# Optimization experiments

Hardware: AMD Instinct MI355X
Metric: run time of the kernel (lower is better)

The kernel has to match this reference:

```python
import jax, jax.numpy as jnp
import numpy as np

G = 8           # graphs
NBG = 1024      # blocks per graph
APB = 4         # atoms per block
NC = 1          # coord channels
HID = 512
ES = 64
K = 9
L = 3
NLVL = 50
NB = G * NBG
NU = NB * APB
NUM_BLOCK, NUM_ATOM, NUM_POS = 25, 16, 16
BIG = 1e9


def _cumsum_ids(seg_lengths, n):
    # faithful to torch: zeros, mark segment starts via cumsum(lengths)[:-1], cumsum
    ids = jnp.zeros((n,), jnp.int32).at[jnp.cumsum(seg_lengths)[:-1]].set(1)
    return jnp.cumsum(ids)


def setup_inputs() -> dict:
    key = jax.random.key(0)
    ks = jax.random.split(key, 18)
    s = 0.02
    return {
        'Z': 3.0 * jax.random.normal(ks[0], (NU, NC, 3), jnp.float32),
        'B': jax.random.randint(ks[1], (NB,), 0, NUM_BLOCK),
        'A': jax.random.randint(ks[2], (NU,), 0, NUM_ATOM),
        'atom_positions': jax.random.randint(ks[3], (NU,), 0, NUM_POS),
        'block_lengths': jnp.full((NB,), APB, jnp.int32),
        'lengths': jnp.full((G,), NBG, jnp.int32),
        'segment_ids': jax.random.randint(ks[4], (NB,), 0, 2),
        'noise': jax.random.normal(ks[5], (NU, NC, 3), jnp.float32),
        'noise_level': jax.random.randint(ks[6], (G,), 0, NLVL),
        'sigmas': jnp.asarray(np.exp(np.linspace(np.log(10.0), np.log(0.01), NLVL)), jnp.float32),
        'atom_emb': s * jax.random.normal(ks[7], (NUM_ATOM, HID), jnp.float32),
        'pos_emb': s * jax.random.normal(ks[8], (NUM_POS, HID), jnp.float32),
        'block_emb': s * jax.random.normal(ks[9], (NUM_BLOCK, HID), jnp.float32),
        'edge_emb': s * jax.random.normal(ks[10], (2, ES), jnp.float32),
        'Wm': s * jax.random.normal(ks[11], (L, HID, HID), jnp.float32),
        'We': s * jax.random.normal(ks[12], (L, ES, HID), jnp.float32),
        'Wu': s * jax.random.normal(ks[13], (L, HID, HID), jnp.float32),
        'wz': s * jax.random.normal(ks[14], (L, HID), jnp.float32),
        'W1': s * jax.random.normal(ks[15], (HID, HID), jnp.float32),
        'b1': jnp.zeros((HID,), jnp.float32),
        'W2': s * jax.random.normal(ks[16], (HID, 1), jnp.float32),
    }


def _forward(Z, B, A, atom_positions, block_lengths, lengths, segment_ids,
             noise, noise_level, sigmas, atom_emb, pos_emb, block_emb, edge_emb,
             Wm, We, Wu, wz, W1, b1, W2):
    nb, nu, g = B.shape[0], A.shape[0], lengths.shape[0]
    nbg, apb = nb // g, nu // nb
    batch_id = _cumsum_ids(lengths, nb)        # [Nb]
    block_id = _cumsum_ids(block_lengths, nu)  # [Nu]

    # perturb: Z + noise * sigma[noise_level[graph]]
    used = sigmas[noise_level][batch_id][block_id]          # [Nu]
    Zp = Z + noise * used[:, None, None]                    # [Nu, NC, 3]

    # block embedding: atom + position + block-type
    H0 = atom_emb[A] + pos_emb[atom_positions] + block_emb[B][block_id]  # [Nu, H]

    # edges: fully connect -> split intra/inter by segment -> knn by min atom-pair distance
    xa = Zp.reshape(g, nbg * apb * NC, 3)
    sq = jnp.sum(xa * xa, axis=-1)
    d2 = sq[:, :, None] + sq[:, None, :] - 2.0 * jnp.einsum('gnd,gmd->gnm', xa, xa)
    D = d2.reshape(g, nbg, apb * NC, nbg, apb * NC).min(axis=(2, 4))     # [g, nbg, nbg]
    seg = segment_ids.reshape(g, nbg)
    same = seg[:, :, None] == seg[:, None, :]
    eye = jnp.eye(nbg, dtype=bool)[None]
    _, idx_intra = jax.lax.top_k(-jnp.where(same & ~eye, D, BIG), K)     # [g, nbg, K]
    _, idx_inter = jax.lax.top_k(-jnp.where(~same, D, BIG), K)
    off = (jnp.arange(g, dtype=jnp.int32) * nbg)[:, None, None]
    dst_loc = jnp.broadcast_to(jnp.arange(nbg, dtype=jnp.int32)[None, :, None] + off, (g, nbg, K))
    src = jnp.concatenate([(idx_intra + off).reshape(-1), (idx_inter + off).reshape(-1)])
    dst = jnp.concatenate([dst_loc.reshape(-1), dst_loc.reshape(-1)])
    eattr = edge_emb[jnp.concatenate([jnp.zeros(g * nbg * K, jnp.int32), jnp.ones(g * nbg * K, jnp.int32)])]

    # encoder (GET surrogate): block-level equivariant message passing
    h = jax.ops.segment_sum(H0, block_id, num_segments=nb) / apb                    # [Nb, H]
    Zb0 = jax.ops.segment_sum(Zp.mean(axis=1), block_id, num_segments=nb) / apb    # [Nb, 3]
    Zb = Zb0
    for l in range(Wm.shape[0]):
        m = jax.nn.silu((h[src] + h[dst]) @ Wm[l] + eattr @ We[l])                  # [E, H]
        h = h + jax.nn.silu(jax.ops.segment_sum(m, dst, num_segments=nb) @ Wu[l])
        coef = jnp.tanh(m @ wz[l])                                                  # [E]
        Zb = Zb + jax.ops.segment_sum((Zb[src] - Zb[dst]) * coef[:, None], dst, num_segments=nb) / (2 * K)
    pred_Z = Zp + (Zb - Zb0)[block_id][:, None, :]
    unit_repr = H0 + h[block_id]
    block_repr = h
    graph_repr = jax.ops.segment_sum(h, batch_id, num_segments=g)

    # energy head: SiLU -> Linear -> SiLU -> Linear(no bias), summed per graph
    e = jax.nn.silu(jax.nn.silu(block_repr) @ W1 + b1) @ W2                         # [Nb, 1]
    pred_energy = jax.ops.segment_sum(e[:, 0], batch_id, num_segments=g)            # [g]

    pred_noise = pred_Z - Zp
    per_unit = jnp.sum((pred_noise - noise) ** 2, axis=(-1, -2))                    # [Nu]
    nl = jax.ops.segment_sum(per_unit, batch_id[block_id], num_segments=g)
    loss = 0.5 * nl.mean()
    return pred_energy, pred_noise, unit_repr, block_repr, graph_repr, loss


def reference(Z, B, A, atom_positions, block_lengths, lengths, segment_ids,
              noise, noise_level, sigmas, atom_emb, pos_emb, block_emb, edge_emb,
              Wm, We, Wu, wz, W1, b1, W2):
    return _forward(Z, B, A, atom_positions, block_lengths, lengths, segment_ids,
                    noise, noise_level, sigmas, atom_emb, pos_emb, block_emb, edge_emb,
                    Wm, We, Wu, wz, W1, b1, W2)
```

## Files before the change

### kernel.cpp

```cpp
#include <hip/hip_runtime.h>
#include <hip/hip_bf16.h>

typedef __bf16 bf16;
typedef __bf16 bf16x2 __attribute__((ext_vector_type(2)));
typedef __bf16 bf16x8 __attribute__((ext_vector_type(8)));
typedef float floatx4 __attribute__((ext_vector_type(4)));

#define NB_ 8192
#define NU_ 32768

__device__ __forceinline__ float silu_f(float x) {
    float e = __expf(-x);
    return x * __builtin_amdgcn_rcpf(1.0f + e);
}

__device__ __forceinline__ float2 unpack_bf2(unsigned v) {
    float2 r;
    r.x = __uint_as_float(v << 16);
    r.y = __uint_as_float(v & 0xFFFF0000u);
    return r;
}

__device__ __forceinline__ void gll16(const bf16* g, bf16* l) {
    __builtin_amdgcn_global_load_lds((const __attribute__((address_space(1))) void*)g,
                                     (__attribute__((address_space(3))) void*)l, 16, 0, 0);
}

__global__ __launch_bounds__(256) void init_kernel(
    const float* __restrict__ Z, const float* __restrict__ noise,
    const int* __restrict__ nl, const float* __restrict__ sig,
    const int* __restrict__ Aarr, const int* __restrict__ posa, const int* __restrict__ Barr,
    const float* __restrict__ atom_emb, const float* __restrict__ pos_emb,
    const float* __restrict__ block_emb,
    const float* __restrict__ edge_emb, const float* __restrict__ We,
    const float* __restrict__ Wm, const float* __restrict__ Wu, const float* __restrict__ W1,
    float* __restrict__ Zp, float* __restrict__ Zb0, float* __restrict__ Zb,
    float* __restrict__ hf, bf16* __restrict__ hb,
    bf16* __restrict__ WmT, bf16* __restrict__ WuT, bf16* __restrict__ W1T,
    float* __restrict__ ebias,
    float* __restrict__ out_gr, float* __restrict__ eblk, float* __restrict__ out_loss)
{
    __shared__ float zsh[12];
    __shared__ float tile[32][33];
    int bid = blockIdx.x, tid = threadIdx.x;
    if (bid < 8192) {
        int b = bid, g = b >> 10;
        if (tid < 12) {
            float sg = sig[nl[g]];
            int idx = b*12 + tid;
            float zp = Z[idx] + noise[idx]*sg;
            Zp[idx] = zp;
            zsh[tid] = zp;
        }
        __syncthreads();
        if (tid < 3) {
            float v = 0.25f*(zsh[tid] + zsh[3+tid] + zsh[6+tid] + zsh[9+tid]);
            Zb0[b*3+tid] = v; Zb[b*3+tid] = v;
        }
        int ai[4], pi[4];
        #pragma unroll
        for (int a = 0; a < 4; a++) { ai[a] = Aarr[b*4+a]*512; pi[a] = posa[b*4+a]*512; }
        int bb = Barr[b]*512;
        #pragma unroll
        for (int cc = 0; cc < 2; cc++) {
            int c = tid + cc*256;
            float s = 0.0f;
            #pragma unroll
            for (int a = 0; a < 4; a++) s += atom_emb[ai[a]+c] + pos_emb[pi[a]+c];
            s = 0.25f*s + block_emb[bb+c];
            hf[(size_t)b*512+c] = s;
            hb[(size_t)b*512+c] = (bf16)s;
        }
        return;
    }
    bid -= 8192;
    if (bid < 1792) {
        int z = bid >> 8, rem = bid & 255;
        int bx = rem & 15, by = rem >> 4;
        int tx = tid & 31, ty = tid >> 5;
        const float* src; bf16* dst;
        if (z < 3)      { src = Wm + (size_t)z*262144;     dst = WmT + (size_t)z*262144; }
        else if (z < 6) { src = Wu + (size_t)(z-3)*262144; dst = WuT + (size_t)(z-3)*262144; }
        else            { src = W1;                        dst = W1T; }
        #pragma unroll
        for (int i = 0; i < 32; i += 8)
            tile[ty+i][tx] = src[(size_t)(by*32+ty+i)*512 + bx*32+tx];
        __syncthreads();
        #pragma unroll
        for (int i = 0; i < 32; i += 8)
            dst[(size_t)(bx*32+ty+i)*512 + by*32+tx] = (bf16)tile[tx][ty+i];
        return;
    }
    bid -= 1792;
    if (bid < 12) {
        int gid = bid*256 + tid;
        int l = gid >> 10, t = (gid >> 9) & 1, c = gid & 511;
        float s = 0.0f;
        #pragma unroll 8
        for (int e = 0; e < 64; e++)
            s += edge_emb[t*64 + e] * We[(size_t)(l*64 + e)*512 + c];
        ebias[gid] = s;
        return;
    }
    bid -= 12;
    int k = bid*256 + tid;
    if (k < 4096) out_gr[k] = 0.0f;
    else if (k < 12288) eblk[k-4096] = 0.0f;
    else if (k == 12288) out_loss[0] = 0.0f;
}

__device__ void knn_body(int kb, const float* __restrict__ Zp, const int* __restrict__ seg,
                         int* __restrict__ nbr) {
    int wid = threadIdx.x >> 6;
    int lane = threadIdx.x & 63;
    int r = ((kb & 7) << 10) + ((kb >> 3) << 2) + wid;
    int g = r >> 10;
    int il = r & 1023;
    int base = g << 10;
    int segr = seg[r];
    float za[4][3];
    #pragma unroll
    for (int a = 0; a < 4; a++)
        #pragma unroll
        for (int d = 0; d < 3; d++)
            za[a][d] = Zp[r*12 + a*3 + d];
    float dist[16];
    unsigned smask = 0;
    #pragma unroll
    for (int t = 0; t < 16; t++) {
        int jb = base + t*64 + lane;
        const float4* p = (const float4*)(Zp + (size_t)jb*12);
        float4 v0 = p[0], v1 = p[1], v2 = p[2];
        float bx[4] = {v0.x, v0.w, v1.z, v2.y};
        float by[4] = {v0.y, v1.x, v1.w, v2.z};
        float bz[4] = {v0.z, v1.y, v2.x, v2.w};
        float dm = 3.0e38f;
        #pragma unroll
        for (int a = 0; a < 4; a++) {
            #pragma unroll
            for (int bq = 0; bq < 4; bq++) {
                float dx = za[a][0]-bx[bq], dy = za[a][1]-by[bq], dz = za[a][2]-bz[bq];
                dm = fminf(dm, dx*dx + dy*dy + dz*dz);
            }
        }
        dist[t] = dm;
        if (seg[jb] == segr) smask |= (1u << t);
    }
    const float INF = 3.0e38f;
    for (int phase = 0; phase < 2; phase++) {
        float wd[16];
        #pragma unroll
        for (int t = 0; t < 16; t++) {
            bool ok = (phase == 0) ? (((smask >> t) & 1u) && (t*64 + lane != il))
                                   : (!((smask >> t) & 1u));
            wd[t] = ok ? dist[t] : INF;
        }
        for (int it = 0; it < 9; it++) {
            float bd = wd[0]; int bt = 0;
            #pragma unroll
            for (int t = 1; t < 16; t++) { if (wd[t] < bd) { bd = wd[t]; bt = t; } }
            float mv = bd;
            #pragma unroll
            for (int off = 32; off >= 1; off >>= 1) mv = fminf(mv, __shfl_xor(mv, off, 64));
            unsigned long long msk = __ballot(bd == mv);
            int wl = __ffsll(msk) - 1;
            int wt = __shfl(bt, wl, 64);
            if (lane == 0) nbr[r*18 + phase*9 + it] = base + wt*64 + wl;
            bool amwin = (lane == wl);
            #pragma unroll
            for (int t = 0; t < 16; t++) if (amwin && t == wt) wd[t] = INF;
        }
    }
}

__device__ void gemm_body(const bf16* __restrict__ A, const bf16* __restrict__ BT,
                          bf16* __restrict__ Pb, float* __restrict__ hf,
                          bf16* __restrict__ hb, bf16* __restrict__ shp,
                          const float* __restrict__ b1, const float* __restrict__ W2,
                          float* __restrict__ eblk,
                          float* __restrict__ Zb, const float* __restrict__ zacc,
                          int mode, int bid)
{
    __shared__ alignas(16) bf16 sA[128*32];
    __shared__ alignas(16) bf16 sB[64*32];
    int mt = bid & 63, nt = bid >> 6;
    int m0 = mt*128, n0 = nt*64;
    int tid = threadIdx.x, lane = tid & 63, w = tid >> 6;
    int wm = w & 1, wn = w >> 1;
    int lm = lane & 15, q = lane >> 4;

    int pA0 = w*128 + lane, pA1 = pA0 + 64, pB = w*64 + lane;
    int rA0 = pA0 >> 2, qA0 = (pA0 & 3) ^ ((rA0 >> 1) & 3);
    int rA1 = pA1 >> 2, qA1 = (pA1 & 3) ^ ((rA1 >> 1) & 3);
    int rB  = pB  >> 2, qB  = (pB  & 3) ^ ((rB  >> 1) & 3);
    const bf16* gA0 = A  + (size_t)(m0 + rA0)*512 + qA0*8;
    const bf16* gA1 = A  + (size_t)(m0 + rA1)*512 + qA1*8;
    const bf16* gB  = BT + (size_t)(n0 + rB )*512 + qB*8;
    bf16* lA0 = sA + (w*128)*8;
    bf16* lA1 = sA + (w*128 + 64)*8;
    bf16* lB  = sB + (w*64)*8;

    int swq = (q ^ ((lm >> 1) & 3)) * 8;
    const bf16* pa[4]; const bf16* pb2[2];
    #pragma unroll
    for (int tm = 0; tm < 4; tm++) pa[tm] = sA + (wm*64 + tm*16 + lm)*32 + swq;
    #pragma unroll
    for (int tn = 0; tn < 2; tn++) pb2[tn] = sB + (wn*32 + tn*16 + lm)*32 + swq;

    floatx4 zv = {0.0f, 0.0f, 0.0f, 0.0f};
    floatx4 acc[4][2];
    #pragma unroll
    for (int i = 0; i < 4; i++)
        #pragma unroll
        for (int j = 0; j < 2; j++) acc[i][j] = zv;

    for (int k0 = 0; k0 < 512; k0 += 32) {
        gll16(gA0 + k0, lA0);
        gll16(gA1 + k0, lA1);
        gll16(gB  + k0, lB);
        __syncthreads();
        bf16x8 af[4], bfr[2];
        #pragma unroll
        for (int tm = 0; tm < 4; tm++) af[tm] = *(const bf16x8*)pa[tm];
        #pragma unroll
        for (int tn = 0; tn < 2; tn++) bfr[tn] = *(const bf16x8*)pb2[tn];
        #pragma unroll
        for (int tm = 0; tm < 4; tm++)
            #pragma unroll
            for (int tn = 0; tn < 2; tn++)
                acc[tm][tn] = __builtin_amdgcn_mfma_f32_16x16x32_bf16(af[tm], bfr[tn], acc[tm][tn], 0, 0, 0);
        __syncthreads();
    }

    if (mode == 1 && nt == 0) {
        int o = m0*3 + tid;
        Zb[o] += zacc[o] * (1.0f/18.0f);
        if (tid < 128) {
            int o2 = m0*3 + 256 + tid;
            Zb[o2] += zacc[o2] * (1.0f/18.0f);
        }
    }

    if (mode == 2) {
        #pragma unroll
        for (int tm = 0; tm < 4; tm++) {
            #pragma unroll
            for (int rr = 0; rr < 4; rr++) {
                float part = 0.0f;
                #pragma unroll
                for (int tn = 0; tn < 2; tn++) {
                    int col = n0 + wn*32 + tn*16 + lm;
                    float t = silu_f(acc[tm][tn][rr] + b1[col]);
                    part += t * W2[col];
                }
                part += __shfl_xor(part, 1, 64);
                part += __shfl_xor(part, 2, 64);
                part += __shfl_xor(part, 4, 64);
                part += __shfl_xor(part, 8, 64);
                if (lm == 0) {
                    int row = m0 + wm*64 + tm*16 + q*4 + rr;
                    atomicAdd(&eblk[row], part);
                }
            }
        }
        return;
    }
    #pragma unroll
    for (int tm = 0; tm < 4; tm++) {
        #pragma unroll
        for (int tn = 0; tn < 2; tn++) {
            #pragma unroll
            for (int rr = 0; rr < 4; rr++) {
                int row = m0 + wm*64 + tm*16 + q*4 + rr;
                int col = n0 + wn*32 + tn*16 + lm;
                size_t o = (size_t)row*512 + col;
                float v = acc[tm][tn][rr];
                if (mode == 0) {
                    Pb[o] = (bf16)v;
                } else {
                    float nh = hf[o] + silu_f(v);
                    hf[o] = nh;
                    hb[o] = (bf16)nh;
                    if (shp) shp[o] = (bf16)silu_f(nh);
                }
            }
        }
    }
}

__global__ __launch_bounds__(256) void gemm_kernel(const bf16* __restrict__ A, const bf16* __restrict__ BT,
                                                   bf16* __restrict__ Pb, float* __restrict__ hf,
                                                   bf16* __restrict__ hb, bf16* __restrict__ shp,
                                                   const float* __restrict__ b1, const float* __restrict__ W2,
                                                   float* __restrict__ eblk,
                                                   float* __restrict__ Zb, const float* __restrict__ zacc,
                                                   int mode) {
    gemm_body(A, BT, Pb, hf, hb, shp, b1, W2, eblk, Zb, zacc, mode, blockIdx.x);
}

__global__ __launch_bounds__(256) void knn_pgemm0_kernel(const bf16* __restrict__ hb,
                                                         const bf16* __restrict__ WmT0,
                                                         bf16* __restrict__ Pb,
                                                         const float* __restrict__ Zp,
                                                         const int* __restrict__ seg,
                                                         int* __restrict__ nbr) {
    if (blockIdx.x < 512)
        gemm_body(hb, WmT0, Pb, nullptr, nullptr, nullptr, nullptr, nullptr, nullptr,
                  nullptr, nullptr, 0, blockIdx.x);
    else
        knn_body(blockIdx.x - 512, Zp, seg, nbr);
}

__global__ __launch_bounds__(256) void edge_kernel(const bf16* __restrict__ Pb, const float* __restrict__ ebias,
                                                   const float* __restrict__ wz, const float* __restrict__ Zb,
                                                   const int* __restrict__ nbr, bf16* __restrict__ msum,
                                                   float* __restrict__ zacc) {
    int bid = blockIdx.x, tid = threadIdx.x;
    int b = ((bid & 7) << 10) | (bid >> 3);
    int c0 = 2*tid;
    int lane = tid & 63, wid = tid >> 6;
    __shared__ int srcs[18];
    __shared__ float red[18][4];
    __shared__ float term[18][3];
    if (tid < 18) srcs[tid] = nbr[b*18 + tid];
    __syncthreads();
    float2 pd  = unpack_bf2(*(const unsigned*)(Pb + (size_t)b*512 + c0));
    float2 eb0 = *(const float2*)(ebias + c0);
    float2 eb1 = *(const float2*)(ebias + 512 + c0);
    float2 w   = *(const float2*)(wz + c0);
    float ms0 = 0.0f, ms1 = 0.0f;
    float pdot[18];
    #pragma unroll
    for (int e = 0; e < 18; e++) {
        int s = srcs[e];
        float2 pv = unpack_bf2(*(const unsigned*)(Pb + (size_t)s*512 + c0));
        float ba = (e < 9) ? eb0.x : eb1.x;
        float bb = (e < 9) ? eb0.y : eb1.y;
        float m0 = silu_f(pv.x + pd.x + ba);
        float m1 = silu_f(pv.y + pd.y + bb);
        ms0 += m0; ms1 += m1;
        pdot[e] = m0*w.x + m1*w.y;
    }
    bf16x2 mp = { (bf16)ms0, (bf16)ms1 };
    *(bf16x2*)(msum + (size_t)b*512 + c0) = mp;
    #pragma unroll
    for (int e = 0; e < 18; e++) {
        float v = pdot[e];
        #pragma unroll
        for (int off = 32; off >= 1; off >>= 1) v += __shfl_xor(v, off, 64);
        if (lane == 0) red[e][wid] = v;
    }
    __syncthreads();
    if (tid < 18) {
        float dot = red[tid][0] + red[tid][1] + red[tid][2] + red[tid][3];
        float coef = tanhf(dot);
        int s = srcs[tid];
        #pragma unroll
        for (int d = 0; d < 3; d++)
            term[tid][d] = (Zb[s*3 + d] - Zb[b*3 + d]) * coef;
    }
    __syncthreads();
    if (tid < 3) {
        float s = 0.0f;
        #pragma unroll
        for (int e = 0; e < 18; e++) s += term[e][tid];
        zacc[b*3 + tid] = s;
    }
}

__global__ __launch_bounds__(256) void finalize_kernel(const float* __restrict__ eblk, float* __restrict__ out_e,
                                                       const float* __restrict__ hf, float* __restrict__ out_gr,
                                                       const float* __restrict__ Zb, const float* __restrict__ Zb0,
                                                       const float* __restrict__ noise,
                                                       float* __restrict__ out_pn, float* __restrict__ out_loss) {
    __shared__ float red[256];
    int bid = blockIdx.x, tid = threadIdx.x;
    if (bid < 8) {
        int g = bid;
        float s = 0.0f;
        #pragma unroll
        for (int k = 0; k < 4; k++) s += eblk[g*1024 + k*256 + tid];
        red[tid] = s; __syncthreads();
        for (int st = 128; st > 0; st >>= 1) {
            if (tid < st) red[tid] += red[tid+st];
            __syncthreads();
        }
        if (tid == 0) out_e[g] = red[0];
        return;
    }
    if (bid < 136) {
        int u = (bid-8)*256 + tid;
        int b = u >> 2;
        float per = 0.0f;
        #pragma unroll
        for (int d = 0; d < 3; d++) {
            float dv = Zb[b*3+d] - Zb0[b*3+d];
            out_pn[u*3+d] = dv;
            float e = dv - noise[u*3+d];
            per += e*e;
        }
        red[tid] = per; __syncthreads();
        for (int st = 128; st > 0; st >>= 1) {
            if (tid < st) red[tid] += red[tid+st];
            __syncthreads();
        }
        if (tid == 0) atomicAdd(out_loss, red[0] * (1.0f/16.0f));
        return;
    }
    int pid = bid - 136;
    int g = pid >> 5;
    int rc = (pid >> 1) & 15;
    int ch = pid & 1;
    int c = ch*256 + tid;
    int b0 = (g << 10) + rc*64;
    float s = 0.0f;
    for (int i = 0; i < 64; i++) s += hf[(size_t)(b0+i)*512 + c];
    atomicAdd(&out_gr[g*512 + c], s);
}

__global__ __launch_bounds__(256) void unitrepr_kernel(const int* __restrict__ Aarr, const int* __restrict__ posa,
                                                       const int* __restrict__ Barr,
                                                       const float* __restrict__ atom_emb, const float* __restrict__ pos_emb,
                                                       const float* __restrict__ block_emb,
                                                       const float* __restrict__ hf, float* __restrict__ out_ur) {
    int gid = blockIdx.x*256 + threadIdx.x;
    int u = gid >> 7, c = (gid & 127) << 2, b = u >> 2;
    float4 va = *(const float4*)(atom_emb + (size_t)Aarr[u]*512 + c);
    float4 vp = *(const float4*)(pos_emb + (size_t)posa[u]*512 + c);
    float4 vb = *(const float4*)(block_emb + (size_t)Barr[b]*512 + c);
    float4 vh = *(const float4*)(hf + (size_t)b*512 + c);
    float4 o;
    o.x = va.x + vp.x + vb.x + vh.x;
    o.y = va.y + vp.y + vb.y + vh.y;
    o.z = va.z + vp.z + vb.z + vh.z;
    o.w = va.w + vp.w + vb.w + vh.w;
    *(float4*)(out_ur + (size_t)u*512 + c) = o;
}

extern "C" void kernel_launch(void* const* d_in, const int* in_sizes, int n_in,
                              void* d_out, int out_size, void* d_ws, size_t ws_size,
                              hipStream_t stream) {
    const float* Z         = (const float*)d_in[0];
    const int*   B         = (const int*)d_in[1];
    const int*   A         = (const int*)d_in[2];
    const int*   ap        = (const int*)d_in[3];
    const int*   seg       = (const int*)d_in[6];
    const float* noise     = (const float*)d_in[7];
    const int*   nl        = (const int*)d_in[8];
    const float* sig       = (const float*)d_in[9];
    const float* atom_emb  = (const float*)d_in[10];
    const float* pos_emb   = (const float*)d_in[11];
    const float* block_emb = (const float*)d_in[12];
    const float* edge_emb  = (const float*)d_in[13];
    const float* Wm        = (const float*)d_in[14];
    const float* We        = (const float*)d_in[15];
    const float* Wu        = (const float*)d_in[16];
    const float* wz        = (const float*)d_in[17];
    const float* W1        = (const float*)d_in[18];
    const float* b1        = (const float*)d_in[19];
    const float* W2        = (const float*)d_in[20];
    (void)in_sizes; (void)n_in; (void)d_ws; (void)ws_size; (void)out_size;

    float* out = (float*)d_out;
    const size_t o1 = 8, o2 = 98312, o3 = 16875528, o4 = 21069832, o5 = 21073928;
    float* out_e    = out;
    float* out_pn   = out + o1;
    float* out_ur   = out + o2;
    float* hf       = out + o3;
    float* out_gr   = out + o4;
    float* out_loss = out + o5;

    char* arena = (char*)(out + o2);
    bf16*  Pb   = (bf16*)(arena);
    bf16*  msum = (bf16*)(arena + 16777216);
    bf16*  sh   = (bf16*)(arena + 25165824);
    bf16*  hb   = (bf16*)(arena + 33554432);
    float* Zp   = (float*)(arena + 41943040);
    float* Zb0  = (float*)(arena + 42336256);
    float* Zb   = (float*)(arena + 42434560);
    float* zacc = (float*)(arena + 42532864);
    int*   nbr  = (int*)  (arena + 42631168);
    bf16*  WmT  = (bf16*) (arena + 43220992);
    bf16*  WuT  = (bf16*) (arena + 44793856);
    bf16*  W1T  = (bf16*) (arena + 46366720);
    float* ebias= (float*)(arena + 46891008);
    float* eblk = (float*)(arena + 46903296);

    init_kernel<<<8192 + 1792 + 12 + 49, 256, 0, stream>>>(
        Z, noise, nl, sig, A, ap, B, atom_emb, pos_emb, block_emb,
        edge_emb, We, Wm, Wu, W1,
        Zp, Zb0, Zb, hf, hb, WmT, WuT, W1T, ebias, out_gr, eblk, out_loss);

    knn_pgemm0_kernel<<<512 + 2048, 256, 0, stream>>>(hb, WmT, Pb, Zp, seg, nbr);

    for (int l = 0; l < 3; l++) {
        if (l > 0)
            gemm_kernel<<<512, 256, 0, stream>>>(hb, WmT + (size_t)l*262144, Pb,
                                                 nullptr, nullptr, nullptr, nullptr, nullptr, nullptr,
                                                 nullptr, nullptr, 0);
        edge_kernel<<<8192, 256, 0, stream>>>(Pb, ebias + l*1024, wz + l*512, Zb, nbr, msum, zacc);
        gemm_kernel<<<512, 256, 0, stream>>>(msum, WuT + (size_t)l*262144, nullptr,
                                             hf, hb, (l == 2) ? sh : nullptr, nullptr, nullptr, nullptr,
                                             Zb, zacc, 1);
    }
    gemm_kernel<<<512, 256, 0, stream>>>(sh, W1T, nullptr, nullptr, nullptr, nullptr,
                                         b1, W2, eblk, nullptr, nullptr, 2);
    finalize_kernel<<<392, 256, 0, stream>>>(eblk, out_e, hf, out_gr, Zb, Zb0, noise, out_pn, out_loss);
    unitrepr_kernel<<<16384, 256, 0, stream>>>(A, ap, B, atom_emb, pos_emb, block_emb, hf, out_ur);
}
```

Measured before the change: 485.1 us.

## Restructure kNN per-row, double-buffer smaller GEMM tiles, fuse energy GEMM with finalize

The kNN search now gives each block a single row. Its four waves each scan a quarter of the candidates using packed distance/index integer keys, and the per-wave top-9 lists are merged through LDS. The GEMM moves to 64x64 tiles with double-buffered global-to-LDS loads and one barrier per k-step, which doubles the grid to 1024 blocks. The energy-head GEMM reduces straight into per-graph energy with one atomic per wave, and is merged with the finalize work so the eblk buffer and its extra launch go away. Init also uses vectorized float2 loads. Risks: the packed keys truncate distance mantissa bits, so tie order can differ from the reference, and kNN now launches 8192 blocks.

```diff
diff --git a/kernel.cpp b/kernel.cpp
--- a/kernel.cpp
+++ b/kernel.cpp
@@ -38,7 +38,7 @@
     float* __restrict__ hf, bf16* __restrict__ hb,
     bf16* __restrict__ WmT, bf16* __restrict__ WuT, bf16* __restrict__ W1T,
     float* __restrict__ ebias,
-    float* __restrict__ out_gr, float* __restrict__ eblk, float* __restrict__ out_loss)
+    float* __restrict__ out_gr, float* __restrict__ out_e, float* __restrict__ out_loss)
 {
     __shared__ float zsh[12];
     __shared__ float tile[32][33];
@@ -61,16 +61,19 @@
         #pragma unroll
         for (int a = 0; a < 4; a++) { ai[a] = Aarr[b*4+a]*512; pi[a] = posa[b*4+a]*512; }
         int bb = Barr[b]*512;
-        #pragma unroll
-        for (int cc = 0; cc < 2; cc++) {
-            int c = tid + cc*256;
-            float s = 0.0f;
-            #pragma unroll
-            for (int a = 0; a < 4; a++) s += atom_emb[ai[a]+c] + pos_emb[pi[a]+c];
-            s = 0.25f*s + block_emb[bb+c];
-            hf[(size_t)b*512+c] = s;
-            hb[(size_t)b*512+c] = (bf16)s;
-        }
+        int c0 = tid*2;
+        float sx = 0.0f, sy = 0.0f;
+        #pragma unroll
+        for (int a = 0; a < 4; a++) {
+            float2 va = *(const float2*)(atom_emb + ai[a] + c0);
+            float2 vp = *(const float2*)(pos_emb + pi[a] + c0);
+            sx += va.x + vp.x; sy += va.y + vp.y;
+        }
+        float2 vb = *(const float2*)(block_emb + bb + c0);
+        sx = 0.25f*sx + vb.x; sy = 0.25f*sy + vb.y;
+        *(float2*)(hf + (size_t)b*512 + c0) = make_float2(sx, sy);
+        bf16x2 hp = { (bf16)sx, (bf16)sy };
+        *(bf16x2*)(hb + (size_t)b*512 + c0) = hp;
         return;
     }
     bid -= 8192;
@@ -105,30 +108,27 @@
     bid -= 12;
     int k = bid*256 + tid;
     if (k < 4096) out_gr[k] = 0.0f;
-    else if (k < 12288) eblk[k-4096] = 0.0f;
-    else if (k == 12288) out_loss[0] = 0.0f;
+    else if (k < 4104) out_e[k-4096] = 0.0f;
+    else if (k == 4104) out_loss[0] = 0.0f;
 }
 
 __device__ void knn_body(int kb, const float* __restrict__ Zp, const int* __restrict__ seg,
-                         int* __restrict__ nbr) {
-    int wid = threadIdx.x >> 6;
-    int lane = threadIdx.x & 63;
-    int r = ((kb & 7) << 10) + ((kb >> 3) << 2) + wid;
-    int g = r >> 10;
-    int il = r & 1023;
+                         int* __restrict__ nbr, unsigned* __restrict__ l1) {
+    int tid = threadIdx.x, w = tid >> 6, lane = tid & 63;
+    int g = kb & 7, rl = kb >> 3;
+    int r = (g << 10) + rl;
     int base = g << 10;
     int segr = seg[r];
-    float za[4][3];
-    #pragma unroll
-    for (int a = 0; a < 4; a++)
-        #pragma unroll
-        for (int d = 0; d < 3; d++)
-            za[a][d] = Zp[r*12 + a*3 + d];
-    float dist[16];
-    unsigned smask = 0;
-    #pragma unroll
-    for (int t = 0; t < 16; t++) {
-        int jb = base + t*64 + lane;
+    const float4* zp4 = (const float4*)(Zp + (size_t)r*12);
+    float4 a0 = zp4[0], a1 = zp4[1], a2 = zp4[2];
+    float ax[4] = {a0.x, a0.w, a1.z, a2.y};
+    float ay[4] = {a0.y, a1.x, a1.w, a2.z};
+    float az[4] = {a0.z, a1.y, a2.x, a2.w};
+    unsigned kin[4], kout[4];
+    #pragma unroll
+    for (int t = 0; t < 4; t++) {
+        int j = w*256 + t*64 + lane;
+        int jb = base + j;
         const float4* p = (const float4*)(Zp + (size_t)jb*12);
         float4 v0 = p[0], v1 = p[1], v2 = p[2];
         float bx[4] = {v0.x, v0.w, v1.z, v2.y};
@@ -139,36 +139,47 @@
         for (int a = 0; a < 4; a++) {
             #pragma unroll
             for (int bq = 0; bq < 4; bq++) {
-                float dx = za[a][0]-bx[bq], dy = za[a][1]-by[bq], dz = za[a][2]-bz[bq];
+                float dx = ax[a]-bx[bq], dy = ay[a]-by[bq], dz = az[a]-bz[bq];
                 dm = fminf(dm, dx*dx + dy*dy + dz*dz);
             }
         }
-        dist[t] = dm;
-        if (seg[jb] == segr) smask |= (1u << t);
-    }
-    const float INF = 3.0e38f;
-    for (int phase = 0; phase < 2; phase++) {
-        float wd[16];
-        #pragma unroll
-        for (int t = 0; t < 16; t++) {
-            bool ok = (phase == 0) ? (((smask >> t) & 1u) && (t*64 + lane != il))
-                                   : (!((smask >> t) & 1u));
-            wd[t] = ok ? dist[t] : INF;
-        }
+        unsigned kd = (__float_as_uint(dm) & 0xFFFFFC00u) | (unsigned)j;
+        bool same = (seg[jb] == segr);
+        kin[t]  = (same && j != rl) ? kd : 0xFFFFFFFFu;
+        kout[t] = (!same)           ? kd : 0xFFFFFFFFu;
+    }
+    if (tid < 128) l1[tid] = 0xFFFFFFFFu;
+    __syncthreads();
+    #pragma unroll
+    for (int ph = 0; ph < 2; ph++) {
+        unsigned wd[4];
+        #pragma unroll
+        for (int t = 0; t < 4; t++) wd[t] = ph ? kout[t] : kin[t];
         for (int it = 0; it < 9; it++) {
-            float bd = wd[0]; int bt = 0;
-            #pragma unroll
-            for (int t = 1; t < 16; t++) { if (wd[t] < bd) { bd = wd[t]; bt = t; } }
-            float mv = bd;
-            #pragma unroll
-            for (int off = 32; off >= 1; off >>= 1) mv = fminf(mv, __shfl_xor(mv, off, 64));
-            unsigned long long msk = __ballot(bd == mv);
-            int wl = __ffsll(msk) - 1;
-            int wt = __shfl(bt, wl, 64);
-            if (lane == 0) nbr[r*18 + phase*9 + it] = base + wt*64 + wl;
-            bool amwin = (lane == wl);
-            #pragma unroll
-            for (int t = 0; t < 16; t++) if (amwin && t == wt) wd[t] = INF;
+            unsigned bk = min(min(wd[0], wd[1]), min(wd[2], wd[3]));
+            unsigned mv = bk;
+            #pragma unroll
+            for (int off = 32; off >= 1; off >>= 1)
+                mv = min(mv, (unsigned)__shfl_xor((int)mv, off, 64));
+            if (lane == 0) l1[ph*64 + w*16 + it] = mv;
+            if (bk == mv) {
+                #pragma unroll
+                for (int t = 0; t < 4; t++) if (wd[t] == mv) wd[t] = 0xFFFFFFFFu;
+            }
+        }
+    }
+    __syncthreads();
+    if (w < 2) {
+        int ph = w;
+        int w2 = lane >> 4, it2 = lane & 15;
+        unsigned key = (it2 < 9) ? l1[ph*64 + w2*16 + it2] : 0xFFFFFFFFu;
+        for (int it = 0; it < 9; it++) {
+            unsigned mv = key;
+            #pragma unroll
+            for (int off = 32; off >= 1; off >>= 1)
+                mv = min(mv, (unsigned)__shfl_xor((int)mv, off, 64));
+            if (key == mv) key = 0xFFFFFFFFu;
+            if (lane == 0) nbr[r*18 + ph*9 + it] = base + (int)(mv & 1023u);
         }
     }
 }
@@ -177,103 +188,85 @@
                           bf16* __restrict__ Pb, float* __restrict__ hf,
                           bf16* __restrict__ hb, bf16* __restrict__ shp,
                           const float* __restrict__ b1, const float* __restrict__ W2,
-                          float* __restrict__ eblk,
+                          float* __restrict__ out_e,
                           float* __restrict__ Zb, const float* __restrict__ zacc,
-                          int mode, int bid)
+                          int mode, int bid, bf16* __restrict__ sA, bf16* __restrict__ sB)
 {
-    __shared__ alignas(16) bf16 sA[128*32];
-    __shared__ alignas(16) bf16 sB[64*32];
-    int mt = bid & 63, nt = bid >> 6;
-    int m0 = mt*128, n0 = nt*64;
+    int mt = bid & 127, nt = bid >> 7;
+    int m0 = mt*64, n0 = nt*64;
     int tid = threadIdx.x, lane = tid & 63, w = tid >> 6;
     int wm = w & 1, wn = w >> 1;
     int lm = lane & 15, q = lane >> 4;
 
-    int pA0 = w*128 + lane, pA1 = pA0 + 64, pB = w*64 + lane;
-    int rA0 = pA0 >> 2, qA0 = (pA0 & 3) ^ ((rA0 >> 1) & 3);
-    int rA1 = pA1 >> 2, qA1 = (pA1 & 3) ^ ((rA1 >> 1) & 3);
-    int rB  = pB  >> 2, qB  = (pB  & 3) ^ ((rB  >> 1) & 3);
-    const bf16* gA0 = A  + (size_t)(m0 + rA0)*512 + qA0*8;
-    const bf16* gA1 = A  + (size_t)(m0 + rA1)*512 + qA1*8;
-    const bf16* gB  = BT + (size_t)(n0 + rB )*512 + qB*8;
-    bf16* lA0 = sA + (w*128)*8;
-    bf16* lA1 = sA + (w*128 + 64)*8;
-    bf16* lB  = sB + (w*64)*8;
-
+    int row = tid >> 2;
+    int qt = (tid & 3) ^ ((row >> 1) & 3);
+    const bf16* gA = A  + (size_t)(m0 + row)*512 + qt*8;
+    const bf16* gB = BT + (size_t)(n0 + row)*512 + qt*8;
+    bf16* lA = sA + tid*8 - lane*8;
+    bf16* lB = sB + tid*8 - lane*8;
     int swq = (q ^ ((lm >> 1) & 3)) * 8;
-    const bf16* pa[4]; const bf16* pb2[2];
-    #pragma unroll
-    for (int tm = 0; tm < 4; tm++) pa[tm] = sA + (wm*64 + tm*16 + lm)*32 + swq;
-    #pragma unroll
-    for (int tn = 0; tn < 2; tn++) pb2[tn] = sB + (wn*32 + tn*16 + lm)*32 + swq;
 
     floatx4 zv = {0.0f, 0.0f, 0.0f, 0.0f};
-    floatx4 acc[4][2];
-    #pragma unroll
-    for (int i = 0; i < 4; i++)
+    floatx4 acc[2][2];
+    #pragma unroll
+    for (int i = 0; i < 2; i++)
         #pragma unroll
         for (int j = 0; j < 2; j++) acc[i][j] = zv;
 
-    for (int k0 = 0; k0 < 512; k0 += 32) {
-        gll16(gA0 + k0, lA0);
-        gll16(gA1 + k0, lA1);
-        gll16(gB  + k0, lB);
+    gll16(gA, lA);
+    gll16(gB, lB);
+    for (int k = 0; k < 16; k++) {
+        int cur = (k & 1)*2048;
         __syncthreads();
-        bf16x8 af[4], bfr[2];
-        #pragma unroll
-        for (int tm = 0; tm < 4; tm++) af[tm] = *(const bf16x8*)pa[tm];
-        #pragma unroll
-        for (int tn = 0; tn < 2; tn++) bfr[tn] = *(const bf16x8*)pb2[tn];
-        #pragma unroll
-        for (int tm = 0; tm < 4; tm++)
+        if (k < 15) {
+            int nxt = ((k+1) & 1)*2048;
+            gll16(gA + (k+1)*32, lA + nxt);
+            gll16(gB + (k+1)*32, lB + nxt);
+        }
+        const bf16* bA = sA + cur;
+        const bf16* bB = sB + cur;
+        bf16x8 af[2], bfr[2];
+        af[0]  = *(const bf16x8*)(bA + (wm*32      + lm)*32 + swq);
+        af[1]  = *(const bf16x8*)(bA + (wm*32 + 16 + lm)*32 + swq);
+        bfr[0] = *(const bf16x8*)(bB + (wn*32      + lm)*32 + swq);
+        bfr[1] = *(const bf16x8*)(bB + (wn*32 + 16 + lm)*32 + swq);
+        #pragma unroll
+        for (int tm = 0; tm < 2; tm++)
             #pragma unroll
             for (int tn = 0; tn < 2; tn++)
                 acc[tm][tn] = __builtin_amdgcn_mfma_f32_16x16x32_bf16(af[tm], bfr[tn], acc[tm][tn], 0, 0, 0);
-        __syncthreads();
-    }
-
-    if (mode == 1 && nt == 0) {
+    }
+
+    if (mode == 2) {
+        float s = 0.0f;
+        #pragma unroll
+        for (int tn = 0; tn < 2; tn++) {
+            int col = n0 + wn*32 + tn*16 + lm;
+            float bb = b1[col], ww = W2[col];
+            #pragma unroll
+            for (int tm = 0; tm < 2; tm++)
+                #pragma unroll
+                for (int rr = 0; rr < 4; rr++)
+                    s += silu_f(acc[tm][tn][rr] + bb) * ww;
+        }
+        #pragma unroll
+        for (int off = 32; off >= 1; off >>= 1) s += __shfl_xor(s, off, 64);
+        if (lane == 0) atomicAdd(&out_e[m0 >> 10], s);
+        return;
+    }
+    if (mode == 1 && nt == 0 && tid < 192) {
         int o = m0*3 + tid;
         Zb[o] += zacc[o] * (1.0f/18.0f);
-        if (tid < 128) {
-            int o2 = m0*3 + 256 + tid;
-            Zb[o2] += zacc[o2] * (1.0f/18.0f);
-        }
-    }
-
-    if (mode == 2) {
-        #pragma unroll
-        for (int tm = 0; tm < 4; tm++) {
+    }
+    #pragma unroll
+    for (int tm = 0; tm < 2; tm++) {
+        #pragma unroll
+        for (int tn = 0; tn < 2; tn++) {
             #pragma unroll
             for (int rr = 0; rr < 4; rr++) {
-                float part = 0.0f;
-                #pragma unroll
-                for (int tn = 0; tn < 2; tn++) {
-                    int col = n0 + wn*32 + tn*16 + lm;
-                    float t = silu_f(acc[tm][tn][rr] + b1[col]);
-                    part += t * W2[col];
-                }
-                part += __shfl_xor(part, 1, 64);
-                part += __shfl_xor(part, 2, 64);
-                part += __shfl_xor(part, 4, 64);
-                part += __shfl_xor(part, 8, 64);
-                if (lm == 0) {
-                    int row = m0 + wm*64 + tm*16 + q*4 + rr;
-                    atomicAdd(&eblk[row], part);
-                }
-            }
-        }
-        return;
-    }
-    #pragma unroll
-    for (int tm = 0; tm < 4; tm++) {
-        #pragma unroll
-        for (int tn = 0; tn < 2; tn++) {
-            #pragma unroll
-            for (int rr = 0; rr < 4; rr++) {
-                int row = m0 + wm*64 + tm*16 + q*4 + rr;
-                int col = n0 + wn*32 + tn*16 + lm;
-                size_t o = (size_t)row*512 + col;
+                int r2 = m0 + wm*32 + tm*16 + q*4 + rr;
+                int c2 = n0 + wn*32 + tn*16 + lm;
+                size_t o = (size_t)r2*512 + c2;
                 float v = acc[tm][tn][rr];
                 if (mode == 0) {
                     Pb[o] = (bf16)v;
@@ -291,11 +284,11 @@
 __global__ __launch_bounds__(256) void gemm_kernel(const bf16* __restrict__ A, const bf16* __restrict__ BT,
                                                    bf16* __restrict__ Pb, float* __restrict__ hf,
                                                    bf16* __restrict__ hb, bf16* __restrict__ shp,
-                                                   const float* __restrict__ b1, const float* __restrict__ W2,
-                                                   float* __restrict__ eblk,
                                                    float* __restrict__ Zb, const float* __restrict__ zacc,
                                                    int mode) {
-    gemm_body(A, BT, Pb, hf, hb, shp, b1, W2, eblk, Zb, zacc, mode, blockIdx.x);
+    __shared__ __align__(16) char smem[16384];
+    gemm_body(A, BT, Pb, hf, hb, shp, nullptr, nullptr, nullptr, Zb, zacc, mode, blockIdx.x,
+              (bf16*)smem, (bf16*)(smem + 8192));
 }
 
 __global__ __launch_bounds__(256) void knn_pgemm0_kernel(const bf16* __restrict__ hb,
@@ -304,11 +297,12 @@
                                                          const float* __restrict__ Zp,
                                                          const int* __restrict__ seg,
                                                          int* __restrict__ nbr) {
-    if (blockIdx.x < 512)
+    __shared__ __align__(16) char smem[16384];
+    if (blockIdx.x < 8192)
+        knn_body(blockIdx.x, Zp, seg, nbr, (unsigned*)smem);
+    else
         gemm_body(hb, WmT0, Pb, nullptr, nullptr, nullptr, nullptr, nullptr, nullptr,
-                  nullptr, nullptr, 0, blockIdx.x);
-    else
-        knn_body(blockIdx.x - 512, Zp, seg, nbr);
+                  nullptr, nullptr, 0, blockIdx.x - 8192, (bf16*)smem, (bf16*)(smem + 8192));
 }
 
 __global__ __launch_bounds__(256) void edge_kernel(const bf16* __restrict__ Pb, const float* __restrict__ ebias,
@@ -368,28 +362,23 @@
     }
 }
 
-__global__ __launch_bounds__(256) void finalize_kernel(const float* __restrict__ eblk, float* __restrict__ out_e,
-                                                       const float* __restrict__ hf, float* __restrict__ out_gr,
-                                                       const float* __restrict__ Zb, const float* __restrict__ Zb0,
-                                                       const float* __restrict__ noise,
-                                                       float* __restrict__ out_pn, float* __restrict__ out_loss) {
-    __shared__ float red[256];
+__global__ __launch_bounds__(256) void egemm_fin_kernel(const bf16* __restrict__ sh, const bf16* __restrict__ W1T,
+                                                        const float* __restrict__ b1, const float* __restrict__ W2,
+                                                        float* __restrict__ out_e,
+                                                        const float* __restrict__ hf, float* __restrict__ out_gr,
+                                                        const float* __restrict__ Zb, const float* __restrict__ Zb0,
+                                                        const float* __restrict__ noise,
+                                                        float* __restrict__ out_pn, float* __restrict__ out_loss) {
+    __shared__ __align__(16) char smem[16384];
     int bid = blockIdx.x, tid = threadIdx.x;
-    if (bid < 8) {
-        int g = bid;
-        float s = 0.0f;
-        #pragma unroll
-        for (int k = 0; k < 4; k++) s += eblk[g*1024 + k*256 + tid];
-        red[tid] = s; __syncthreads();
-        for (int st = 128; st > 0; st >>= 1) {
-            if (tid < st) red[tid] += red[tid+st];
-            __syncthreads();
-        }
-        if (tid == 0) out_e[g] = red[0];
-        return;
-    }
-    if (bid < 136) {
-        int u = (bid-8)*256 + tid;
+    if (bid < 1024) {
+        gemm_body(sh, W1T, nullptr, nullptr, nullptr, nullptr, b1, W2, out_e,
+                  nullptr, nullptr, 2, bid, (bf16*)smem, (bf16*)(smem + 8192));
+        return;
+    }
+    float* red = (float*)smem;
+    if (bid < 1152) {
+        int u = (bid-1024)*256 + tid;
         int b = u >> 2;
         float per = 0.0f;
         #pragma unroll
@@ -407,7 +396,7 @@
         if (tid == 0) atomicAdd(out_loss, red[0] * (1.0f/16.0f));
         return;
     }
-    int pid = bid - 136;
+    int pid = bid - 1152;
     int g = pid >> 5;
     int rc = (pid >> 1) & 15;
     int ch = pid & 1;
@@ -484,27 +473,23 @@
     bf16*  WuT  = (bf16*) (arena + 44793856);
     bf16*  W1T  = (bf16*) (arena + 46366720);
     float* ebias= (float*)(arena + 46891008);
-    float* eblk = (float*)(arena + 46903296);
-
-    init_kernel<<<8192 + 1792 + 12 + 49, 256, 0, stream>>>(
+
+    init_kernel<<<8192 + 1792 + 12 + 17, 256, 0, stream>>>(
         Z, noise, nl, sig, A, ap, B, atom_emb, pos_emb, block_emb,
         edge_emb, We, Wm, Wu, W1,
-        Zp, Zb0, Zb, hf, hb, WmT, WuT, W1T, ebias, out_gr, eblk, out_loss);
-
-    knn_pgemm0_kernel<<<512 + 2048, 256, 0, stream>>>(hb, WmT, Pb, Zp, seg, nbr);
+        Zp, Zb0, Zb, hf, hb, WmT, WuT, W1T, ebias, out_gr, out_e, out_loss);
+
+    knn_pgemm0_kernel<<<8192 + 1024, 256, 0, stream>>>(hb, WmT, Pb, Zp, seg, nbr);
 
     for (int l = 0; l < 3; l++) {
         if (l > 0)
-            gemm_kernel<<<512, 256, 0, stream>>>(hb, WmT + (size_t)l*262144, Pb,
-                                                 nullptr, nullptr, nullptr, nullptr, nullptr, nullptr,
-                                                 nullptr, nullptr, 0);
+            gemm_kernel<<<1024, 256, 0, stream>>>(hb, WmT + (size_t)l*262144, Pb,
+                                                  nullptr, nullptr, nullptr, nullptr, nullptr, 0);
         edge_kernel<<<8192, 256, 0, stream>>>(Pb, ebias + l*1024, wz + l*512, Zb, nbr, msum, zacc);
-        gemm_kernel<<<512, 256, 0, stream>>>(msum, WuT + (size_t)l*262144, nullptr,
-                                             hf, hb, (l == 2) ? sh : nullptr, nullptr, nullptr, nullptr,
-                                             Zb, zacc, 1);
-    }
-    gemm_kernel<<<512, 256, 0, stream>>>(sh, W1T, nullptr, nullptr, nullptr, nullptr,
-                                         b1, W2, eblk, nullptr, nullptr, 2);
-    finalize_kernel<<<392, 256, 0, stream>>>(eblk, out_e, hf, out_gr, Zb, Zb0, noise, out_pn, out_loss);
+        gemm_kernel<<<1024, 256, 0, stream>>>(msum, WuT + (size_t)l*262144, nullptr,
+                                              hf, hb, (l == 2) ? sh : nullptr, Zb, zacc, 1);
+    }
+    egemm_fin_kernel<<<1024 + 128 + 256, 256, 0, stream>>>(sh, W1T, b1, W2, out_e,
+                                                           hf, out_gr, Zb, Zb0, noise, out_pn, out_loss);
     unitrepr_kernel<<<16384, 256, 0, stream>>>(A, ap, B, atom_emb, pos_emb, block_emb, hf, out_ur);
 }
```

Result: slower. 530.2 us (+9.3%).
